# Optimization experiments

Measured on AMD Instinct MI355X. Metric: run time of the kernel, lower is better.

Reference implementation:

```python
import jax, jax.numpy as jnp
import numpy as np

WINDOW_SIZE = 11
SIGMA = 1.5
C1 = 0.01 ** 2
C2 = 0.03 ** 2


def _gaussian_window(window_size, sigma, channel):
    x = np.arange(window_size, dtype=np.float64)
    g = np.exp(-((x - window_size // 2) ** 2) / (2.0 * sigma ** 2))
    g = g / g.sum()
    w2d = np.outer(g, g).astype(np.float32)  # [K,K]
    # depthwise kernel: [C, 1, K, K] (OIHW with feature_group_count=C)
    return jnp.asarray(np.broadcast_to(w2d, (channel, 1, window_size, window_size)).copy())


def _depthwise_blur(x, window):
    pad = WINDOW_SIZE // 2
    return jax.lax.conv_general_dilated(
        x, window,
        window_strides=(1, 1),
        padding=[(pad, pad), (pad, pad)],
        feature_group_count=x.shape[1],
        dimension_numbers=('NCHW', 'OIHW', 'NCHW'))


def setup_inputs() -> dict:
    key = jax.random.key(0)
    k1, k2 = jax.random.split(key)
    shape = (16, 3, 512, 512)
    image = jax.random.uniform(k1, shape, dtype=jnp.float32)
    target = jax.random.uniform(k2, shape, dtype=jnp.float32)
    return {"image": image, "target": target}


def reference(image, target):
    channel = image.shape[1]
    window = _gaussian_window(WINDOW_SIZE, SIGMA, channel)

    mu1 = _depthwise_blur(image, window)
    mu2 = _depthwise_blur(target, window)
    mu1_sq = mu1 * mu1
    mu2_sq = mu2 * mu2
    mu1_mu2 = mu1 * mu2

    sigma1_sq = _depthwise_blur(image * image, window) - mu1_sq
    sigma2_sq = _depthwise_blur(target * target, window) - mu2_sq
    sigma12 = _depthwise_blur(image * target, window) - mu1_mu2

    ssim_map = ((2.0 * mu1_mu2 + C1) * (2.0 * sigma12 + C2)) / (
        (mu1_sq + mu2_sq + C1) * (sigma1_sq + sigma2_sq + C2))
    return 1.0 - jnp.mean(ssim_map)
```

## Files before the change

### kernel.cpp

```cpp
#include <hip/hip_runtime.h>
#include <hip/hip_fp16.h>
#include <math.h>


#define HH 512
#define WW 512
#define NPLANES 48
#define G_TILES 8
#define NBLOCKS 768

typedef _Float16 f16x8 __attribute__((ext_vector_type(8)));
typedef _Float16 f16x4 __attribute__((ext_vector_type(4)));
typedef float f32x4 __attribute__((ext_vector_type(4)));

#define RAW_STRIDE 208
#define RAW_PLANE  9984
#define OUTH_CSTR  104
#define LDS_TOTAL  39936

struct WParam { float A, B; };

__global__ void ssim_init_out(float* out) { out[0] = 1.0f; }

__global__ __launch_bounds__(256, 4)
void ssim_mfma(const float* __restrict__ img, const float* __restrict__ tgt,
               float* __restrict__ out, WParam wp) {
    __shared__ alignas(16) char lds[LDS_TOTAL];
    __shared__ float wsum[4];

    const int tid  = threadIdx.x;
    const int wid  = tid >> 6;
    const int lane = tid & 63;
    const int cl   = lane & 15;
    const int am   = lane >> 4;

    for (int i = tid; i < LDS_TOTAL / 4; i += 256)
        ((float*)lds)[i] = 0.f;

    f16x8 Bh, Av;
    #pragma unroll
    for (int j = 0; j < 8; ++j) {
        int k = 8 * am + j;
        int ih = k - cl - 3;
        float th = (float)(ih - 5);
        Bh[j] = ((unsigned)ih <= 10u) ? (_Float16)(wp.A * exp2f(-wp.B * th * th))
                                      : (_Float16)0.f;
        int iv = k - cl;
        float tv = (float)(iv - 5);
        Av[j] = ((unsigned)iv <= 10u) ? (_Float16)(wp.A * exp2f(-wp.B * tv * tv))
                                      : (_Float16)0.f;
    }
    __syncthreads();

    const float C1 = 1e-4f, C2 = 9e-4f;
    float lsum = 0.f;

    for (int g = 0; g < G_TILES; ++g) {
        const int tlin = blockIdx.x * G_TILES + g;
        const int p    = tlin >> 7;
        const int rem  = tlin & 127;
        const int R0   = (rem >> 3) * 32;
        const int C0   = (rem & 7) * 64;
        const float* ip = img + (size_t)p * (HH * WW);
        const float* tp = tgt + (size_t)p * (HH * WW);

        for (int it = tid; it < 420; it += 256) {
            int r   = it / 10;
            int grp = it - r * 10;
            int gr  = R0 - 5 + r;
            int gc0 = C0 - 8 + grp * 8;
            float4 xa = make_float4(0.f,0.f,0.f,0.f), xb = xa, ya = xa, yb = xa;
            if ((unsigned)gr < (unsigned)HH) {
                const float* xr = ip + (size_t)gr * WW;
                const float* yr = tp + (size_t)gr * WW;
                if ((unsigned)gc0 <= (unsigned)(WW - 4)) {
                    xa = *(const float4*)(xr + gc0);
                    ya = *(const float4*)(yr + gc0);
                }
                if ((unsigned)(gc0 + 4) <= (unsigned)(WW - 4)) {
                    xb = *(const float4*)(xr + gc0 + 4);
                    yb = *(const float4*)(yr + gc0 + 4);
                }
            }
            float fx[8] = {xa.x,xa.y,xa.z,xa.w, xb.x,xb.y,xb.z,xb.w};
            float fy[8] = {ya.x,ya.y,ya.z,ya.w, yb.x,yb.y,yb.z,yb.w};
            f16x8 hx, hy, hs, hp;
            #pragma unroll
            for (int j = 0; j < 8; ++j) {
                hx[j] = (_Float16)fx[j];
                hy[j] = (_Float16)fy[j];
                hs[j] = (_Float16)fmaf(fx[j], fx[j], fy[j]*fy[j]);
                hp[j] = (_Float16)(fx[j] * fy[j]);
            }
            char* base = lds + r * RAW_STRIDE + grp * 16;
            *(f16x8*)(base + 0*RAW_PLANE) = hx;
            *(f16x8*)(base + 1*RAW_PLANE) = hy;
            *(f16x8*)(base + 2*RAW_PLANE) = hs;
            *(f16x8*)(base + 3*RAW_PLANE) = hp;
        }
        __syncthreads();

        {
            char* plane = lds + wid * RAW_PLANE;
            const int abase = cl * RAW_STRIDE + am * 16;
            f16x8 Af[3][4];
            #pragma unroll
            for (int mt = 0; mt < 3; ++mt)
                #pragma unroll
                for (int nt = 0; nt < 4; ++nt)
                    Af[mt][nt] = *(const f16x8*)(plane + abase
                                                 + mt * 16 * RAW_STRIDE + nt * 32);
            __builtin_amdgcn_sched_barrier(0);
            const int wbase = cl * OUTH_CSTR + am * 8;
            #pragma unroll
            for (int nt = 0; nt < 4; ++nt) {
                #pragma unroll
                for (int mt = 0; mt < 3; ++mt) {
                    f32x4 acc = {0.f, 0.f, 0.f, 0.f};
                    acc = __builtin_amdgcn_mfma_f32_16x16x32_f16(
                              Af[mt][nt], Bh, acc, 0, 0, 0);
                    f16x4 h;
                    #pragma unroll
                    for (int j = 0; j < 4; ++j) h[j] = (_Float16)acc[j];
                    *(f16x4*)(plane + wbase + nt * 16 * OUTH_CSTR + mt * 32) = h;
                }
            }
        }
        __syncthreads();

        {
            const int bbase = (16 * wid + cl) * OUTH_CSTR + am * 16;
            f32x4 accv[4][2];
            #pragma unroll
            for (int q = 0; q < 4; ++q) {
                #pragma unroll
                for (int mt = 0; mt < 2; ++mt) {
                    f16x8 Bf = *(const f16x8*)(lds + q * RAW_PLANE + bbase + mt * 32);
                    f32x4 acc = {0.f, 0.f, 0.f, 0.f};
                    accv[q][mt] = __builtin_amdgcn_mfma_f32_16x16x32_f16(
                                      Av, Bf, acc, 0, 0, 0);
                }
            }
            #pragma unroll
            for (int mt = 0; mt < 2; ++mt) {
                #pragma unroll
                for (int j = 0; j < 4; ++j) {
                    float mu1 = accv[0][mt][j], mu2 = accv[1][mt][j];
                    float bss = accv[2][mt][j], bxy = accv[3][mt][j];
                    float mu1s = mu1*mu1, mu2s = mu2*mu2, mu12 = mu1*mu2;
                    float ssum = bss - mu1s - mu2s;
                    float s12  = bxy - mu12;
                    float num = (2.f*mu12 + C1) * (2.f*s12 + C2);
                    float den = (mu1s + mu2s + C1) * (ssum + C2);
                    lsum = fmaf(num, __builtin_amdgcn_rcpf(den), lsum);
                }
            }
        }
        __syncthreads();
    }

    for (int off = 32; off > 0; off >>= 1)
        lsum += __shfl_down(lsum, off, 64);
    if (lane == 0) wsum[wid] = lsum;
    __syncthreads();
    if (tid == 0) {
        float bsum = wsum[0] + wsum[1] + wsum[2] + wsum[3];
        const float invN = 1.0f / (float)((size_t)NPLANES * HH * WW);
        atomicAdd(out, -bsum * invN);
    }
}

extern "C" void kernel_launch(void* const* d_in, const int* in_sizes, int n_in,
                              void* d_out, int out_size, void* d_ws, size_t ws_size,
                              hipStream_t stream) {
    const float* img = (const float*)d_in[0];
    const float* tgt = (const float*)d_in[1];
    float* out = (float*)d_out;

    double s = 0.0;
    for (int i = 0; i < 11; ++i) {
        double d = (double)(i - 5);
        s += exp(-(d * d) / 4.5);
    }
    WParam wp;
    wp.A = (float)(1.0 / s);
    wp.B = (float)(M_LOG2E / 4.5);

    ssim_init_out<<<1, 1, 0, stream>>>(out);
    ssim_mfma<<<NBLOCKS, 256, 0, stream>>>(img, tgt, out, wp);
}
```

Measured before the change: 45.13 us.

## Prefetch next tile into registers and use barriers that skip draining global loads

The global loads for tile g+1 are issued into registers right after tile g is written to LDS, so they overlap the two MFMA passes. __syncthreads is replaced by a barrier that waits only on LDS counters, so outstanding global loads are not drained at each barrier. The squared-sum and product terms are now computed in packed fp16 from the already-converted values rather than in fp32 with one rounding at the end. This adds register pressure under launch_bounds(256,4) and loses some precision in the x*x+y*y and x*y terms.

```diff
diff --git a/kernel.cpp b/kernel.cpp
--- a/kernel.cpp
+++ b/kernel.cpp
@@ -22,6 +22,12 @@
 
 __global__ void ssim_init_out(float* out) { out[0] = 1.0f; }
 
+__device__ __forceinline__ void barrier_nodrain() {
+    asm volatile("s_waitcnt lgkmcnt(0)" ::: "memory");
+    __builtin_amdgcn_s_barrier();
+    __builtin_amdgcn_sched_barrier(0);
+}
+
 __global__ __launch_bounds__(256, 4)
 void ssim_mfma(const float* __restrict__ img, const float* __restrict__ tgt,
                float* __restrict__ out, WParam wp) {
@@ -33,6 +39,72 @@
     const int lane = tid & 63;
     const int cl   = lane & 15;
     const int am   = lane >> 4;
+
+    const int it0 = tid,       ir0 = it0 / 10, ig0 = it0 - 10 * ir0;
+    const int it1 = tid + 256, ir1 = it1 / 10, ig1 = it1 - 10 * ir1;
+    const bool has1 = (tid < 164);
+
+    float4 Xa[2], Xb[2], Ya[2], Yb[2];
+
+    auto load_tile = [&](int tlin) {
+        const int p   = tlin >> 7;
+        const int rem = tlin & 127;
+        const int R0  = (rem >> 3) * 32;
+        const int C0  = (rem & 7) * 64;
+        const float* ip = img + (size_t)p * (HH * WW);
+        const float* tp = tgt + (size_t)p * (HH * WW);
+        #pragma unroll
+        for (int s = 0; s < 2; ++s) {
+            if (s == 1 && !has1) break;
+            int r   = s ? ir1 : ir0;
+            int grp = s ? ig1 : ig0;
+            int gr  = R0 - 5 + r;
+            int gc0 = C0 - 8 + grp * 8;
+            float4 xa = make_float4(0.f,0.f,0.f,0.f), xb = xa, ya = xa, yb = xa;
+            if ((unsigned)gr < (unsigned)HH) {
+                const float* xr = ip + (size_t)gr * WW;
+                const float* yr = tp + (size_t)gr * WW;
+                if ((unsigned)gc0 <= (unsigned)(WW - 4)) {
+                    xa = *(const float4*)(xr + gc0);
+                    ya = *(const float4*)(yr + gc0);
+                }
+                if ((unsigned)(gc0 + 4) <= (unsigned)(WW - 4)) {
+                    xb = *(const float4*)(xr + gc0 + 4);
+                    yb = *(const float4*)(yr + gc0 + 4);
+                }
+            }
+            Xa[s] = xa; Xb[s] = xb; Ya[s] = ya; Yb[s] = yb;
+        }
+    };
+
+    auto write_tile = [&]() {
+        #pragma unroll
+        for (int s = 0; s < 2; ++s) {
+            if (s == 1 && !has1) break;
+            int r   = s ? ir1 : ir0;
+            int grp = s ? ig1 : ig0;
+            float fx[8] = {Xa[s].x,Xa[s].y,Xa[s].z,Xa[s].w,
+                           Xb[s].x,Xb[s].y,Xb[s].z,Xb[s].w};
+            float fy[8] = {Ya[s].x,Ya[s].y,Ya[s].z,Ya[s].w,
+                           Yb[s].x,Yb[s].y,Yb[s].z,Yb[s].w};
+            f16x8 hx, hy;
+            #pragma unroll
+            for (int j = 0; j < 8; ++j) {
+                hx[j] = (_Float16)fx[j];
+                hy[j] = (_Float16)fy[j];
+            }
+            f16x8 hs = hx*hx + hy*hy;
+            f16x8 hp = hx*hy;
+            char* base = lds + r * RAW_STRIDE + grp * 16;
+            *(f16x8*)(base + 0*RAW_PLANE) = hx;
+            *(f16x8*)(base + 1*RAW_PLANE) = hy;
+            *(f16x8*)(base + 2*RAW_PLANE) = hs;
+            *(f16x8*)(base + 3*RAW_PLANE) = hp;
+        }
+    };
+
+    const int base_t = blockIdx.x * G_TILES;
+    load_tile(base_t);
 
     for (int i = tid; i < LDS_TOTAL / 4; i += 256)
         ((float*)lds)[i] = 0.f;
@@ -56,49 +128,9 @@
     float lsum = 0.f;
 
     for (int g = 0; g < G_TILES; ++g) {
-        const int tlin = blockIdx.x * G_TILES + g;
-        const int p    = tlin >> 7;
-        const int rem  = tlin & 127;
-        const int R0   = (rem >> 3) * 32;
-        const int C0   = (rem & 7) * 64;
-        const float* ip = img + (size_t)p * (HH * WW);
-        const float* tp = tgt + (size_t)p * (HH * WW);
-
-        for (int it = tid; it < 420; it += 256) {
-            int r   = it / 10;
-            int grp = it - r * 10;
-            int gr  = R0 - 5 + r;
-            int gc0 = C0 - 8 + grp * 8;
-            float4 xa = make_float4(0.f,0.f,0.f,0.f), xb = xa, ya = xa, yb = xa;
-            if ((unsigned)gr < (unsigned)HH) {
-                const float* xr = ip + (size_t)gr * WW;
-                const float* yr = tp + (size_t)gr * WW;
-                if ((unsigned)gc0 <= (unsigned)(WW - 4)) {
-                    xa = *(const float4*)(xr + gc0);
-                    ya = *(const float4*)(yr + gc0);
-                }
-                if ((unsigned)(gc0 + 4) <= (unsigned)(WW - 4)) {
-                    xb = *(const float4*)(xr + gc0 + 4);
-                    yb = *(const float4*)(yr + gc0 + 4);
-                }
-            }
-            float fx[8] = {xa.x,xa.y,xa.z,xa.w, xb.x,xb.y,xb.z,xb.w};
-            float fy[8] = {ya.x,ya.y,ya.z,ya.w, yb.x,yb.y,yb.z,yb.w};
-            f16x8 hx, hy, hs, hp;
-            #pragma unroll
-            for (int j = 0; j < 8; ++j) {
-                hx[j] = (_Float16)fx[j];
-                hy[j] = (_Float16)fy[j];
-                hs[j] = (_Float16)fmaf(fx[j], fx[j], fy[j]*fy[j]);
-                hp[j] = (_Float16)(fx[j] * fy[j]);
-            }
-            char* base = lds + r * RAW_STRIDE + grp * 16;
-            *(f16x8*)(base + 0*RAW_PLANE) = hx;
-            *(f16x8*)(base + 1*RAW_PLANE) = hy;
-            *(f16x8*)(base + 2*RAW_PLANE) = hs;
-            *(f16x8*)(base + 3*RAW_PLANE) = hp;
-        }
-        __syncthreads();
+        write_tile();
+        if (g + 1 < G_TILES) load_tile(base_t + g + 1);
+        barrier_nodrain();
 
         {
             char* plane = lds + wid * RAW_PLANE;
@@ -126,7 +158,7 @@
                 }
             }
         }
-        __syncthreads();
+        barrier_nodrain();
 
         {
             const int bbase = (16 * wid + cl) * OUTH_CSTR + am * 16;
@@ -156,7 +188,7 @@
                 }
             }
         }
-        __syncthreads();
+        barrier_nodrain();
     }
 
     for (int off = 32; off > 0; off >>= 1)
```

Result: faster. 40.73 us (-9.8%).

## Keep separable blur entirely in registers, drop LDS staging and barriers

Applied to the files above, without the earlier changes.

Each wave now loads its own 16-column strip of image and target straight from global memory into MFMA A-operand registers. The horizontal pass result is fed directly into the vertical pass by reusing the accumulator layout as B operands for 16x16x16 MFMAs, so the LDS buffers and all intra-tile __syncthreads are removed. The squared and product terms are now computed in fp16 rather than fp32, and the grid changes to 1024 blocks of 6 tiles. This trades LDS traffic and barrier stalls for redundant halo loads from global/L2 and slightly lower precision for the squared terms.

```diff
diff --git a/kernel.cpp b/kernel.cpp
--- a/kernel.cpp
+++ b/kernel.cpp
@@ -5,27 +5,29 @@
 
 #define HH 512
 #define WW 512
+#define HW (HH*WW)
 #define NPLANES 48
-#define G_TILES 8
-#define NBLOCKS 768
+#define G_TILES 6
+#define NBLOCKS 1024
 
 typedef _Float16 f16x8 __attribute__((ext_vector_type(8)));
 typedef _Float16 f16x4 __attribute__((ext_vector_type(4)));
 typedef float f32x4 __attribute__((ext_vector_type(4)));
 
-#define RAW_STRIDE 208
-#define RAW_PLANE  9984
-#define OUTH_CSTR  104
-#define LDS_TOTAL  39936
-
 struct WParam { float A, B; };
 
 __global__ void ssim_init_out(float* out) { out[0] = 1.0f; }
 
+__device__ __forceinline__ f16x8 cvt8(float4 a, float4 b) {
+    f16x8 h;
+    h[0]=(_Float16)a.x; h[1]=(_Float16)a.y; h[2]=(_Float16)a.z; h[3]=(_Float16)a.w;
+    h[4]=(_Float16)b.x; h[5]=(_Float16)b.y; h[6]=(_Float16)b.z; h[7]=(_Float16)b.w;
+    return h;
+}
+
 __global__ __launch_bounds__(256, 4)
 void ssim_mfma(const float* __restrict__ img, const float* __restrict__ tgt,
                float* __restrict__ out, WParam wp) {
-    __shared__ alignas(16) char lds[LDS_TOTAL];
     __shared__ float wsum[4];
 
     const int tid  = threadIdx.x;
@@ -34,23 +36,27 @@
     const int cl   = lane & 15;
     const int am   = lane >> 4;
 
-    for (int i = tid; i < LDS_TOTAL / 4; i += 256)
-        ((float*)lds)[i] = 0.f;
-
-    f16x8 Bh, Av;
+    f16x8 Bh;
     #pragma unroll
     for (int j = 0; j < 8; ++j) {
-        int k = 8 * am + j;
-        int ih = k - cl - 3;
-        float th = (float)(ih - 5);
-        Bh[j] = ((unsigned)ih <= 10u) ? (_Float16)(wp.A * exp2f(-wp.B * th * th))
-                                      : (_Float16)0.f;
-        int iv = k - cl;
-        float tv = (float)(iv - 5);
-        Av[j] = ((unsigned)iv <= 10u) ? (_Float16)(wp.A * exp2f(-wp.B * tv * tv))
+        int ih = 8*am + j - cl - 3;
+        float t = (float)(ih - 5);
+        Bh[j] = ((unsigned)ih <= 10u) ? (_Float16)(wp.A * exp2f(-wp.B*t*t))
                                       : (_Float16)0.f;
     }
-    __syncthreads();
+    f16x4 Av1, Av2;
+    #pragma unroll
+    for (int j = 0; j < 4; ++j) {
+        int k = 4*am + j;
+        int i1 = k - cl;
+        float t1 = (float)(i1 - 5);
+        Av1[j] = ((unsigned)i1 <= 10u) ? (_Float16)(wp.A * exp2f(-wp.B*t1*t1))
+                                       : (_Float16)0.f;
+        int i2 = k + 16 - cl;
+        float t2 = (float)(i2 - 5);
+        Av2[j] = ((unsigned)i2 <= 10u) ? (_Float16)(wp.A * exp2f(-wp.B*t2*t2))
+                                       : (_Float16)0.f;
+    }
 
     const float C1 = 1e-4f, C2 = 9e-4f;
     float lsum = 0.f;
@@ -61,102 +67,87 @@
         const int rem  = tlin & 127;
         const int R0   = (rem >> 3) * 32;
         const int C0   = (rem & 7) * 64;
-        const float* ip = img + (size_t)p * (HH * WW);
-        const float* tp = tgt + (size_t)p * (HH * WW);
+        const float* ip = img + (size_t)p * HW;
+        const float* tp = tgt + (size_t)p * HW;
+        const int cw   = C0 + 16*wid;
+        const int colb = cw - 8 + 8*am;
 
-        for (int it = tid; it < 420; it += 256) {
-            int r   = it / 10;
-            int grp = it - r * 10;
-            int gr  = R0 - 5 + r;
-            int gc0 = C0 - 8 + grp * 8;
-            float4 xa = make_float4(0.f,0.f,0.f,0.f), xb = xa, ya = xa, yb = xa;
-            if ((unsigned)gr < (unsigned)HH) {
-                const float* xr = ip + (size_t)gr * WW;
-                const float* yr = tp + (size_t)gr * WW;
-                if ((unsigned)gc0 <= (unsigned)(WW - 4)) {
-                    xa = *(const float4*)(xr + gc0);
-                    ya = *(const float4*)(yr + gc0);
-                }
-                if ((unsigned)(gc0 + 4) <= (unsigned)(WW - 4)) {
-                    xb = *(const float4*)(xr + gc0 + 4);
-                    yb = *(const float4*)(yr + gc0 + 4);
-                }
+        f16x8 hx[3], hy[3];
+        const bool edge = (R0 == 0) | (R0 == 480) | (cw == 0) | (cw == 496);
+        if (!edge) {
+            #pragma unroll
+            for (int mt = 0; mt < 3; ++mt) {
+                int r = R0 - 5 + 16*mt + cl;
+                const float* xr = ip + (size_t)r * WW + colb;
+                const float* yr = tp + (size_t)r * WW + colb;
+                float4 x0 = *(const float4*)(xr);
+                float4 x1 = *(const float4*)(xr + 4);
+                float4 y0 = *(const float4*)(yr);
+                float4 y1 = *(const float4*)(yr + 4);
+                hx[mt] = cvt8(x0, x1);
+                hy[mt] = cvt8(y0, y1);
             }
-            float fx[8] = {xa.x,xa.y,xa.z,xa.w, xb.x,xb.y,xb.z,xb.w};
-            float fy[8] = {ya.x,ya.y,ya.z,ya.w, yb.x,yb.y,yb.z,yb.w};
-            f16x8 hx, hy, hs, hp;
+        } else {
+            const bool cv0 = (unsigned)colb <= 508u;
+            const bool cv1 = (unsigned)(colb + 4) <= 508u;
+            const int cb0 = cv0 ? colb : 0;
+            const int cb1 = cv1 ? colb + 4 : 0;
+            const float4 z = make_float4(0.f, 0.f, 0.f, 0.f);
             #pragma unroll
-            for (int j = 0; j < 8; ++j) {
-                hx[j] = (_Float16)fx[j];
-                hy[j] = (_Float16)fy[j];
-                hs[j] = (_Float16)fmaf(fx[j], fx[j], fy[j]*fy[j]);
-                hp[j] = (_Float16)(fx[j] * fy[j]);
-            }
-            char* base = lds + r * RAW_STRIDE + grp * 16;
-            *(f16x8*)(base + 0*RAW_PLANE) = hx;
-            *(f16x8*)(base + 1*RAW_PLANE) = hy;
-            *(f16x8*)(base + 2*RAW_PLANE) = hs;
-            *(f16x8*)(base + 3*RAW_PLANE) = hp;
-        }
-        __syncthreads();
-
-        {
-            char* plane = lds + wid * RAW_PLANE;
-            const int abase = cl * RAW_STRIDE + am * 16;
-            f16x8 Af[3][4];
-            #pragma unroll
-            for (int mt = 0; mt < 3; ++mt)
-                #pragma unroll
-                for (int nt = 0; nt < 4; ++nt)
-                    Af[mt][nt] = *(const f16x8*)(plane + abase
-                                                 + mt * 16 * RAW_STRIDE + nt * 32);
-            __builtin_amdgcn_sched_barrier(0);
-            const int wbase = cl * OUTH_CSTR + am * 8;
-            #pragma unroll
-            for (int nt = 0; nt < 4; ++nt) {
-                #pragma unroll
-                for (int mt = 0; mt < 3; ++mt) {
-                    f32x4 acc = {0.f, 0.f, 0.f, 0.f};
-                    acc = __builtin_amdgcn_mfma_f32_16x16x32_f16(
-                              Af[mt][nt], Bh, acc, 0, 0, 0);
-                    f16x4 h;
-                    #pragma unroll
-                    for (int j = 0; j < 4; ++j) h[j] = (_Float16)acc[j];
-                    *(f16x4*)(plane + wbase + nt * 16 * OUTH_CSTR + mt * 32) = h;
-                }
+            for (int mt = 0; mt < 3; ++mt) {
+                int r = R0 - 5 + 16*mt + cl;
+                bool rv = (unsigned)r < (unsigned)HH;
+                size_t ro = (size_t)(rv ? r : 0) * WW;
+                const float* xr = ip + ro;
+                const float* yr = tp + ro;
+                float4 x0 = (rv && cv0) ? *(const float4*)(xr + cb0) : z;
+                float4 x1 = (rv && cv1) ? *(const float4*)(xr + cb1) : z;
+                float4 y0 = (rv && cv0) ? *(const float4*)(yr + cb0) : z;
+                float4 y1 = (rv && cv1) ? *(const float4*)(yr + cb1) : z;
+                hx[mt] = cvt8(x0, x1);
+                hy[mt] = cvt8(y0, y1);
             }
         }
-        __syncthreads();
 
-        {
-            const int bbase = (16 * wid + cl) * OUTH_CSTR + am * 16;
-            f32x4 accv[4][2];
+        f32x4 Dh[4][3];
+        #pragma unroll
+        for (int mt = 0; mt < 3; ++mt) {
+            f16x8 hs = hx[mt]*hx[mt] + hy[mt]*hy[mt];
+            f16x8 hp = hx[mt]*hy[mt];
+            f32x4 zz = {0.f, 0.f, 0.f, 0.f};
+            Dh[0][mt] = __builtin_amdgcn_mfma_f32_16x16x32_f16(hx[mt], Bh, zz, 0, 0, 0);
+            Dh[1][mt] = __builtin_amdgcn_mfma_f32_16x16x32_f16(hy[mt], Bh, zz, 0, 0, 0);
+            Dh[2][mt] = __builtin_amdgcn_mfma_f32_16x16x32_f16(hs,     Bh, zz, 0, 0, 0);
+            Dh[3][mt] = __builtin_amdgcn_mfma_f32_16x16x32_f16(hp,     Bh, zz, 0, 0, 0);
+        }
+
+        #pragma unroll
+        for (int mtv = 0; mtv < 2; ++mtv) {
+            f32x4 accv[4];
             #pragma unroll
             for (int q = 0; q < 4; ++q) {
+                f16x4 B1, B2;
                 #pragma unroll
-                for (int mt = 0; mt < 2; ++mt) {
-                    f16x8 Bf = *(const f16x8*)(lds + q * RAW_PLANE + bbase + mt * 32);
-                    f32x4 acc = {0.f, 0.f, 0.f, 0.f};
-                    accv[q][mt] = __builtin_amdgcn_mfma_f32_16x16x32_f16(
-                                      Av, Bf, acc, 0, 0, 0);
+                for (int j = 0; j < 4; ++j) {
+                    B1[j] = (_Float16)Dh[q][mtv][j];
+                    B2[j] = (_Float16)Dh[q][mtv+1][j];
                 }
+                f32x4 zz = {0.f, 0.f, 0.f, 0.f};
+                f32x4 acc = __builtin_amdgcn_mfma_f32_16x16x16f16(Av2, B2, zz, 0, 0, 0);
+                accv[q]   = __builtin_amdgcn_mfma_f32_16x16x16f16(Av1, B1, acc, 0, 0, 0);
             }
             #pragma unroll
-            for (int mt = 0; mt < 2; ++mt) {
-                #pragma unroll
-                for (int j = 0; j < 4; ++j) {
-                    float mu1 = accv[0][mt][j], mu2 = accv[1][mt][j];
-                    float bss = accv[2][mt][j], bxy = accv[3][mt][j];
-                    float mu1s = mu1*mu1, mu2s = mu2*mu2, mu12 = mu1*mu2;
-                    float ssum = bss - mu1s - mu2s;
-                    float s12  = bxy - mu12;
-                    float num = (2.f*mu12 + C1) * (2.f*s12 + C2);
-                    float den = (mu1s + mu2s + C1) * (ssum + C2);
-                    lsum = fmaf(num, __builtin_amdgcn_rcpf(den), lsum);
-                }
+            for (int j = 0; j < 4; ++j) {
+                float mu1 = accv[0][j], mu2 = accv[1][j];
+                float bss = accv[2][j], bxy = accv[3][j];
+                float mu1s = mu1*mu1, mu2s = mu2*mu2, mu12 = mu1*mu2;
+                float ssum = bss - mu1s - mu2s;
+                float s12  = bxy - mu12;
+                float num = (2.f*mu12 + C1) * (2.f*s12 + C2);
+                float den = (mu1s + mu2s + C1) * (ssum + C2);
+                lsum = fmaf(num, __builtin_amdgcn_rcpf(den), lsum);
             }
         }
-        __syncthreads();
     }
 
     for (int off = 32; off > 0; off >>= 1)
```

New measurement: 133.0 us. +194.7%, slower.
